# Kernel tuning notes

Hardware: AMD Instinct MI355X
Metric: run time of the kernel (lower is better)

The kernel has to match this reference:

```python
import jax, jax.numpy as jnp
from jax import lax
import numpy as np

B, C, H, W = 16, 1, 1024, 1024


def _erode(x, ksize=3):
    # torch: zero-pad then min over ksize x ksize window
    pad = (ksize - 1) // 2
    xp = jnp.pad(x, ((0, 0), (0, 0), (pad, pad), (pad, pad)))  # constant 0, matches F.pad
    return lax.reduce_window(xp, jnp.array(jnp.inf, x.dtype), lax.min,
                             (1, 1, ksize, ksize), (1, 1, 1, 1), 'VALID')


def _circle_weights(y_true):
    e1 = _erode(y_true)
    e2 = _erode(e1)
    e3 = _erode(e2)
    e4 = _erode(e3)
    circle_all = (0.4 * (y_true - e1) + 0.5 * (e1 - e2)
                  + 0.6 * (e2 - e3) + 0.7 * (e3 - e4))
    circle_all = jnp.where(circle_all == 0, jnp.asarray(0.8, circle_all.dtype), circle_all)
    return lax.stop_gradient(circle_all)  # computed under torch.no_grad()


def setup_inputs() -> dict:
    key = jax.random.key(0)
    k1, k2 = jax.random.split(key)
    y_pred = jax.random.uniform(k1, (B, C, H, W), dtype=jnp.float32)
    # binary-ish segmentation mask so erosion rings are non-trivial
    y_true = (jax.random.uniform(k2, (B, C, H, W)) > 0.7).astype(jnp.float32)
    return {"y_pred": y_pred, "y_true": y_true}


def reference(y_pred, y_true):
    w = _circle_weights(y_true)
    loss = (y_pred - y_true) ** 2 * w  # MSELoss(reduction='none') * weights
    return (loss.mean(axis=(1, 2, 3)), loss.mean())
```

## Files before the change

kernel.cpp:

```cpp
#include <hip/hip_runtime.h>
#include <stdint.h>

#define BATCH 16
#define HH 1024
#define WW 1024
#define TH 8
#define HALO 4
#define ROWS (TH + 2*HALO)
#define WORDS (WW/64)
#define NTHREADS 256
#define NWAVES (NTHREADS/64)
#define TOTAL_WORDS (BATCH * HH * WORDS)

__global__ __launch_bounds__(NTHREADS) void pack_kernel(
    const float* __restrict__ y_true,
    unsigned long long* __restrict__ packed)
{
    const int lane = threadIdx.x & 63;
    const size_t base = ((size_t)((blockIdx.x * NTHREADS + threadIdx.x) >> 6)) * 64;
    unsigned long long mine = 0ull;
    #pragma unroll 16
    for (int i = 0; i < 64; ++i) {
        float v = y_true[(base + (size_t)i) * 64 + lane];
        unsigned long long m = __ballot(v != 0.0f);
        mine = (lane == i) ? m : mine;
    }
    packed[base + lane] = mine;
}

__global__ __launch_bounds__(NTHREADS) void erode_mse_kernel(
    const float* __restrict__ y_pred,
    const unsigned long long* __restrict__ packed,
    float* __restrict__ out)
{
    __shared__ unsigned long long bits0[ROWS][WORDS];
    __shared__ unsigned long long bufA[ROWS][WORDS];
    __shared__ unsigned long long bufB[ROWS][WORDS];
    __shared__ unsigned long long E[4][TH][WORDS];
    __shared__ float wavesum[NWAVES];

    const int tid  = threadIdx.x;
    const int lane = tid & 63;
    const int wave = tid >> 6;

    const int im = blockIdx.x / (HH / TH);
    const int rb = blockIdx.x % (HH / TH);
    const int r0 = rb * TH - HALO;

    const float* yp = y_pred + (size_t)im * HH * WW;

    {
        int row  = tid >> 4;
        int word = tid & (WORDS - 1);
        int gr   = r0 + row;
        unsigned long long m = 0ull;
        if (gr >= 0 && gr < HH)
            m = packed[((size_t)im * HH + gr) * WORDS + word];
        bits0[row][word] = m;
        bufA[row][word]  = m;
    }
    __syncthreads();

    #pragma unroll
    for (int k = 1; k <= 4; ++k) {
        unsigned long long (*src)[WORDS] = (k & 1) ? bufA : bufB;
        unsigned long long (*dst)[WORDS] = (k & 1) ? bufB : bufA;
        int lo = k, hi = ROWS - k;
        int n  = (hi - lo) * WORDS;
        if (tid < n) {
            int row  = lo + (tid >> 4);
            int word = tid & (WORDS - 1);
            unsigned long long h0, h1, h2;
            {
                unsigned long long m = src[row - 1][word];
                unsigned long long l = (word > 0)         ? src[row - 1][word - 1] : 0ull;
                unsigned long long r = (word < WORDS - 1) ? src[row - 1][word + 1] : 0ull;
                h0 = m & ((m << 1) | (l >> 63)) & ((m >> 1) | (r << 63));
            }
            {
                unsigned long long m = src[row][word];
                unsigned long long l = (word > 0)         ? src[row][word - 1] : 0ull;
                unsigned long long r = (word < WORDS - 1) ? src[row][word + 1] : 0ull;
                h1 = m & ((m << 1) | (l >> 63)) & ((m >> 1) | (r << 63));
            }
            {
                unsigned long long m = src[row + 1][word];
                unsigned long long l = (word > 0)         ? src[row + 1][word - 1] : 0ull;
                unsigned long long r = (word < WORDS - 1) ? src[row + 1][word + 1] : 0ull;
                h2 = m & ((m << 1) | (l >> 63)) & ((m >> 1) | (r << 63));
            }
            unsigned long long res = h0 & h1 & h2;
            dst[row][word] = res;
            if (row >= HALO && row < HALO + TH) E[k - 1][row - HALO][word] = res;
        }
        __syncthreads();
    }

    const int word = tid >> 4;
    const int bsh  = (tid & 15) * 4;
    float lsum = 0.0f;
    #pragma unroll
    for (int row = 0; row < TH; ++row) {
        int gr = r0 + HALO + row;
        float4 pv = *reinterpret_cast<const float4*>(&yp[(size_t)gr * WW + tid * 4]);
        unsigned int y4 = (unsigned int)((bits0[row + HALO][word] >> bsh) & 0xFull);
        unsigned int n1 = (unsigned int)((E[0][row][word] >> bsh) & 0xFull);
        unsigned int n2 = (unsigned int)((E[1][row][word] >> bsh) & 0xFull);
        unsigned int n3 = (unsigned int)((E[2][row][word] >> bsh) & 0xFull);
        unsigned int n4 = (unsigned int)((E[3][row][word] >> bsh) & 0xFull);
        float pvals[4] = {pv.x, pv.y, pv.z, pv.w};
        #pragma unroll
        for (int j = 0; j < 4; ++j) {
            unsigned int y = (y4 >> j) & 1u;
            unsigned int c = y + ((n1 >> j) & 1u) + ((n2 >> j) & 1u)
                               + ((n3 >> j) & 1u) + ((n4 >> j) & 1u);
            float w = (c == 0u || c == 5u) ? 0.8f : (0.3f + 0.1f * (float)c);
            float d = pvals[j] - (float)y;
            lsum += d * d * w;
        }
    }

    for (int off = 32; off > 0; off >>= 1)
        lsum += __shfl_down(lsum, off, 64);
    if (lane == 0) wavesum[wave] = lsum;
    __syncthreads();
    if (tid == 0) {
        float s = 0.0f;
        for (int wv = 0; wv < NWAVES; ++wv) s += wavesum[wv];
        atomicAdd(&out[im], s * (1.0f / (float)(HH * WW)));
        atomicAdd(&out[BATCH], s * (1.0f / ((float)BATCH * (float)(HH * WW))));
    }
}

__global__ __launch_bounds__(NTHREADS) void circle_mse_kernel(
    const float* __restrict__ y_pred,
    const float* __restrict__ y_true,
    float* __restrict__ out)
{
    __shared__ unsigned long long bits0[ROWS][WORDS];
    __shared__ unsigned long long cur[ROWS][WORDS];
    __shared__ unsigned long long tmp[ROWS][WORDS];
    __shared__ unsigned long long E[4][TH][WORDS];
    __shared__ float wavesum[NWAVES];

    const int tid  = threadIdx.x;
    const int lane = tid & 63;
    const int wave = tid >> 6;
    const int im = blockIdx.x / (HH / TH);
    const int rb = blockIdx.x % (HH / TH);
    const int r0 = rb * TH - HALO;
    const float* yt = y_true + (size_t)im * HH * WW;
    const float* yp = y_pred + (size_t)im * HH * WW;

    #pragma unroll 8
    for (int p = wave; p < ROWS * WORDS; p += NWAVES) {
        int row  = p >> 4;
        int word = p & (WORDS - 1);
        int gr   = r0 + row;
        unsigned long long m = 0ull;
        if (gr >= 0 && gr < HH) {
            float v = yt[(size_t)gr * WW + word * 64 + lane];
            m = __ballot(v != 0.0f);
        }
        if (lane == 0) { bits0[row][word] = m; cur[row][word] = m; }
    }
    __syncthreads();

    for (int k = 1; k <= 4; ++k) {
        int lo = k - 1, hi = ROWS - (k - 1);
        for (int p = tid; p < (hi - lo) * WORDS; p += NTHREADS) {
            int row  = lo + (p >> 4);
            int word = p & (WORDS - 1);
            unsigned long long m = cur[row][word];
            unsigned long long l = (word > 0)         ? cur[row][word - 1] : 0ull;
            unsigned long long r = (word < WORDS - 1) ? cur[row][word + 1] : 0ull;
            tmp[row][word] = m & ((m << 1) | (l >> 63)) & ((m >> 1) | (r << 63));
        }
        __syncthreads();
        lo = k; hi = ROWS - k;
        for (int p = tid; p < (hi - lo) * WORDS; p += NTHREADS) {
            int row  = lo + (p >> 4);
            int word = p & (WORDS - 1);
            unsigned long long res = tmp[row - 1][word] & tmp[row][word] & tmp[row + 1][word];
            cur[row][word] = res;
            if (row >= HALO && row < HALO + TH) E[k - 1][row - HALO][word] = res;
        }
        __syncthreads();
    }

    const int word = tid >> 4;
    const int bsh  = (tid & 15) * 4;
    float lsum = 0.0f;
    #pragma unroll
    for (int row = 0; row < TH; ++row) {
        int gr = r0 + HALO + row;
        float4 pv = *reinterpret_cast<const float4*>(&yp[(size_t)gr * WW + tid * 4]);
        unsigned int y4 = (unsigned int)((bits0[row + HALO][word] >> bsh) & 0xFull);
        unsigned int n1 = (unsigned int)((E[0][row][word] >> bsh) & 0xFull);
        unsigned int n2 = (unsigned int)((E[1][row][word] >> bsh) & 0xFull);
        unsigned int n3 = (unsigned int)((E[2][row][word] >> bsh) & 0xFull);
        unsigned int n4 = (unsigned int)((E[3][row][word] >> bsh) & 0xFull);
        float pvals[4] = {pv.x, pv.y, pv.z, pv.w};
        #pragma unroll
        for (int j = 0; j < 4; ++j) {
            unsigned int y = (y4 >> j) & 1u;
            unsigned int c = y + ((n1 >> j) & 1u) + ((n2 >> j) & 1u)
                               + ((n3 >> j) & 1u) + ((n4 >> j) & 1u);
            float w = (c == 0u || c == 5u) ? 0.8f : (0.3f + 0.1f * (float)c);
            float d = pvals[j] - (float)y;
            lsum += d * d * w;
        }
    }
    for (int off = 32; off > 0; off >>= 1)
        lsum += __shfl_down(lsum, off, 64);
    if (lane == 0) wavesum[wave] = lsum;
    __syncthreads();
    if (tid == 0) {
        float s = 0.0f;
        for (int wv = 0; wv < NWAVES; ++wv) s += wavesum[wv];
        atomicAdd(&out[im], s * (1.0f / (float)(HH * WW)));
        atomicAdd(&out[BATCH], s * (1.0f / ((float)BATCH * (float)(HH * WW))));
    }
}

extern "C" void kernel_launch(void* const* d_in, const int* in_sizes, int n_in,
                              void* d_out, int out_size, void* d_ws, size_t ws_size,
                              hipStream_t stream) {
    const float* y_pred = (const float*)d_in[0];
    const float* y_true = (const float*)d_in[1];
    float* out = (float*)d_out;

    hipMemsetAsync(d_out, 0, (size_t)out_size * sizeof(float), stream);

    const size_t need = (size_t)TOTAL_WORDS * sizeof(unsigned long long);
    if (ws_size >= need && d_ws != nullptr) {
        unsigned long long* packed = (unsigned long long*)d_ws;
        pack_kernel<<<dim3(TOTAL_WORDS / 64 / NWAVES), NTHREADS, 0, stream>>>(y_true, packed);
        erode_mse_kernel<<<dim3(BATCH * (HH / TH)), NTHREADS, 0, stream>>>(y_pred, packed, out);
    } else {
        circle_mse_kernel<<<dim3(BATCH * (HH / TH)), NTHREADS, 0, stream>>>(y_pred, y_true, out);
    }
}
```

Before: 169.1 us.

## Replace atomics with partial-sum reduce kernel, halve pack work per wave, pad LDS

Result: faster. 148.8 us (-12.0%).

```diff
diff --git a/kernel.cpp b/kernel.cpp
--- a/kernel.cpp
+++ b/kernel.cpp
@@ -8,35 +8,37 @@
 #define HALO 4
 #define ROWS (TH + 2*HALO)
 #define WORDS (WW/64)
+#define WPAD (WORDS + 1)
 #define NTHREADS 256
 #define NWAVES (NTHREADS/64)
 #define TOTAL_WORDS (BATCH * HH * WORDS)
+#define NBLOCKS_MSE (BATCH * (HH / TH))
 
 __global__ __launch_bounds__(NTHREADS) void pack_kernel(
     const float* __restrict__ y_true,
     unsigned long long* __restrict__ packed)
 {
     const int lane = threadIdx.x & 63;
-    const size_t base = ((size_t)((blockIdx.x * NTHREADS + threadIdx.x) >> 6)) * 64;
+    const size_t base = ((size_t)((blockIdx.x * NTHREADS + threadIdx.x) >> 6)) * 32;
     unsigned long long mine = 0ull;
-    #pragma unroll 16
-    for (int i = 0; i < 64; ++i) {
+    #pragma unroll
+    for (int i = 0; i < 32; ++i) {
         float v = y_true[(base + (size_t)i) * 64 + lane];
         unsigned long long m = __ballot(v != 0.0f);
         mine = (lane == i) ? m : mine;
     }
-    packed[base + lane] = mine;
+    if (lane < 32) packed[base + lane] = mine;
 }
 
 __global__ __launch_bounds__(NTHREADS) void erode_mse_kernel(
     const float* __restrict__ y_pred,
     const unsigned long long* __restrict__ packed,
-    float* __restrict__ out)
-{
-    __shared__ unsigned long long bits0[ROWS][WORDS];
-    __shared__ unsigned long long bufA[ROWS][WORDS];
-    __shared__ unsigned long long bufB[ROWS][WORDS];
-    __shared__ unsigned long long E[4][TH][WORDS];
+    float* __restrict__ ws_partial)
+{
+    __shared__ unsigned long long bits0[ROWS][WPAD];
+    __shared__ unsigned long long bufA[ROWS][WPAD];
+    __shared__ unsigned long long bufB[ROWS][WPAD];
+    __shared__ unsigned long long E[4][TH][WPAD];
     __shared__ float wavesum[NWAVES];
 
     const int tid  = threadIdx.x;
@@ -63,8 +65,8 @@
 
     #pragma unroll
     for (int k = 1; k <= 4; ++k) {
-        unsigned long long (*src)[WORDS] = (k & 1) ? bufA : bufB;
-        unsigned long long (*dst)[WORDS] = (k & 1) ? bufB : bufA;
+        unsigned long long (*src)[WPAD] = (k & 1) ? bufA : bufB;
+        unsigned long long (*dst)[WPAD] = (k & 1) ? bufB : bufA;
         int lo = k, hi = ROWS - k;
         int n  = (hi - lo) * WORDS;
         if (tid < n) {
@@ -127,8 +129,37 @@
     if (tid == 0) {
         float s = 0.0f;
         for (int wv = 0; wv < NWAVES; ++wv) s += wavesum[wv];
-        atomicAdd(&out[im], s * (1.0f / (float)(HH * WW)));
-        atomicAdd(&out[BATCH], s * (1.0f / ((float)BATCH * (float)(HH * WW))));
+        ws_partial[blockIdx.x] = s;
+    }
+}
+
+__global__ __launch_bounds__(NTHREADS) void reduce_kernel(
+    const float* __restrict__ partial,
+    float* __restrict__ out)
+{
+    __shared__ float ssum[NTHREADS];
+    __shared__ float imsum[BATCH];
+    const int tid = threadIdx.x;
+    float s = 0.0f;
+    #pragma unroll
+    for (int j = 0; j < NBLOCKS_MSE / NTHREADS; ++j)
+        s += partial[tid * (NBLOCKS_MSE / NTHREADS) + j];
+    ssum[tid] = s;
+    __syncthreads();
+    if (tid < BATCH) {
+        float a = 0.0f;
+        #pragma unroll
+        for (int t = 0; t < NTHREADS / BATCH; ++t)
+            a += ssum[tid * (NTHREADS / BATCH) + t];
+        imsum[tid] = a;
+        out[tid] = a * (1.0f / (float)(HH * WW));
+    }
+    __syncthreads();
+    if (tid == 0) {
+        float tot = 0.0f;
+        #pragma unroll
+        for (int i = 0; i < BATCH; ++i) tot += imsum[i];
+        out[BATCH] = tot * (1.0f / ((float)BATCH * (float)(HH * WW)));
     }
 }
 
@@ -137,10 +168,10 @@
     const float* __restrict__ y_true,
     float* __restrict__ out)
 {
-    __shared__ unsigned long long bits0[ROWS][WORDS];
-    __shared__ unsigned long long cur[ROWS][WORDS];
-    __shared__ unsigned long long tmp[ROWS][WORDS];
-    __shared__ unsigned long long E[4][TH][WORDS];
+    __shared__ unsigned long long bits0[ROWS][WPAD];
+    __shared__ unsigned long long cur[ROWS][WPAD];
+    __shared__ unsigned long long tmp[ROWS][WPAD];
+    __shared__ unsigned long long E[4][TH][WPAD];
     __shared__ float wavesum[NWAVES];
 
     const int tid  = threadIdx.x;
@@ -230,14 +261,16 @@
     const float* y_true = (const float*)d_in[1];
     float* out = (float*)d_out;
 
-    hipMemsetAsync(d_out, 0, (size_t)out_size * sizeof(float), stream);
-
-    const size_t need = (size_t)TOTAL_WORDS * sizeof(unsigned long long);
+    const size_t need = (size_t)TOTAL_WORDS * sizeof(unsigned long long)
+                      + (size_t)NBLOCKS_MSE * sizeof(float);
     if (ws_size >= need && d_ws != nullptr) {
         unsigned long long* packed = (unsigned long long*)d_ws;
-        pack_kernel<<<dim3(TOTAL_WORDS / 64 / NWAVES), NTHREADS, 0, stream>>>(y_true, packed);
-        erode_mse_kernel<<<dim3(BATCH * (HH / TH)), NTHREADS, 0, stream>>>(y_pred, packed, out);
+        float* ws_partial = (float*)(packed + TOTAL_WORDS);
+        pack_kernel<<<dim3(TOTAL_WORDS / 32 / NWAVES), NTHREADS, 0, stream>>>(y_true, packed);
+        erode_mse_kernel<<<dim3(NBLOCKS_MSE), NTHREADS, 0, stream>>>(y_pred, packed, ws_partial);
+        reduce_kernel<<<dim3(1), NTHREADS, 0, stream>>>(ws_partial, out);
     } else {
-        circle_mse_kernel<<<dim3(BATCH * (HH / TH)), NTHREADS, 0, stream>>>(y_pred, y_true, out);
-    }
-}
+        hipMemsetAsync(d_out, 0, (size_t)out_size * sizeof(float), stream);
+        circle_mse_kernel<<<dim3(NBLOCKS_MSE), NTHREADS, 0, stream>>>(y_pred, y_true, out);
+    }
+}
```
